# Performance work log

Hardware: AMD Instinct MI355X
Metric: run time of the kernel (lower is better)

The kernel has to match this reference:

```python
import jax, jax.numpy as jnp
import numpy as np

VOC = 50000
EMB = 300
B = 256
CTX = 6
K = 10


def setup_inputs() -> dict:
    key = jax.random.key(0)
    k1, k2, k3, k4, k5, k6 = jax.random.split(key, 6)
    # one-hot inputs (the original multiplies one-hot vectors against the tables)
    idx_vo = jax.random.randint(k1, (B,), 0, VOC)
    idx_vi = jax.random.randint(k2, (B, CTX), 0, VOC)
    idx_neg = jax.random.randint(k3, (B, K), 0, VOC)
    # random context lengths in [1, CTX]; positions >= length are zero rows (padding)
    lengths = jax.random.randint(k4, (B, 1), 1, CTX + 1)
    valid = (jnp.arange(CTX)[None, :] < lengths).astype(jnp.float32)  # [B, CTX]
    vo = jax.nn.one_hot(idx_vo, VOC, dtype=jnp.float32)               # [B, VOC]
    vi = jax.nn.one_hot(idx_vi, VOC, dtype=jnp.float32) * valid[:, :, None]  # [B, CTX, VOC]
    neg_samples = jax.nn.one_hot(idx_neg, VOC, dtype=jnp.float32)     # [B, K, VOC]
    # parameters: uniform(-0.5, 0.5) / embed_dim, as in the torch init
    V = (jax.random.uniform(k5, (VOC, EMB), minval=-0.5, maxval=0.5) / EMB).astype(jnp.float32)
    U = (jax.random.uniform(k6, (VOC, EMB), minval=-0.5, maxval=0.5) / EMB).astype(jnp.float32)
    return {"vo": vo, "vi": vi, "neg_samples": neg_samples, "V": V, "U": U}


def reference(vo, vi, neg_samples, V, U):
    embed_dim = V.shape[1]
    vo_embed = vo @ V                                      # [B, D]
    vi_temp = jnp.einsum('bcv,vd->bcd', vi, U)             # [B, CTX, D]
    mask = jnp.sum(jnp.abs(vi), axis=2) != 0               # [B, CTX]
    mask_sum = mask.astype(jnp.float32).sum(axis=1, keepdims=True)  # [B, 1]
    vi_embed = vi_temp.sum(axis=1) / mask_sum              # [B, D]
    left = jax.nn.log_sigmoid(jnp.sum(vo_embed * vi_embed, axis=1, keepdims=True))  # [B, 1]
    neg_embed = jnp.einsum('bkv,vd->bkd', neg_samples, U)  # [B, K, D]
    batch_mul = jnp.einsum('bkd,bd->bk', neg_embed, vo_embed)  # [B, K]
    right = jnp.sum(jax.nn.log_sigmoid(-batch_mul), axis=1, keepdims=True)  # [B, 1]
    return jnp.mean(-(left + right))
```

## Files before the change

kernel.cpp:

```cpp
#include <hip/hip_runtime.h>
#include <math.h>

#define VOC 50000
#define EMB 300
#define BSZ 256
#define CTX 6
#define KNEG 10
#define ROW_VECS (VOC / 4)
#define NROWS (BSZ + BSZ * CTX + BSZ * KNEG)

typedef float floatx4 __attribute__((ext_vector_type(4)));

__global__ __launch_bounds__(256) void scan_rows_kernel(
        const floatx4* __restrict__ vo,
        const floatx4* __restrict__ vi,
        const floatx4* __restrict__ neg,
        int* __restrict__ out_idx,
        float* __restrict__ out) {
    const int r = blockIdx.x;
    if (r == 0 && threadIdx.x == 0) *out = 0.0f;

    const floatx4* __restrict__ row;
    if (r < BSZ)                 row = vo  + (size_t)r * ROW_VECS;
    else if (r < BSZ + BSZ*CTX)  row = vi  + (size_t)(r - BSZ) * ROW_VECS;
    else                         row = neg + (size_t)(r - BSZ - BSZ*CTX) * ROW_VECS;

    __shared__ int found;
    if (threadIdx.x == 0) found = 0;
    __syncthreads();

    const int t = threadIdx.x;
    for (int base = 0; base < ROW_VECS; base += 1024) {
        floatx4 v[4];
        int     j[4];
#pragma unroll
        for (int u = 0; u < 4; ++u) {
            j[u] = base + u * 256 + t;
            if (j[u] < ROW_VECS) v[u] = __builtin_nontemporal_load(&row[j[u]]);
            else                 v[u] = (floatx4)(0.f, 0.f, 0.f, 0.f);
        }
#pragma unroll
        for (int u = 0; u < 4; ++u) {
            if (v[u].x != 0.0f || v[u].y != 0.0f || v[u].z != 0.0f || v[u].w != 0.0f) {
                int col = j[u] * 4;
                if (v[u].x != 0.0f)      col += 0;
                else if (v[u].y != 0.0f) col += 1;
                else if (v[u].z != 0.0f) col += 2;
                else                     col += 3;
                out_idx[r] = col;
                found = 1;
            }
        }
        __syncthreads();
        if (found) return;
        __syncthreads();
    }
    if (t == 0) out_idx[r] = -1;
}

__device__ __forceinline__ float log_sigmoid(float x) {
    return fminf(x, 0.0f) - log1pf(expf(-fabsf(x)));
}

__global__ void cbow_loss_kernel(const int* __restrict__ idx_vo,
                                 const int* __restrict__ idx_vi,
                                 const int* __restrict__ idx_neg,
                                 const float* __restrict__ V,
                                 const float* __restrict__ U,
                                 float* __restrict__ out) {
    const int b = blockIdx.x;
    const int lane = threadIdx.x;

    const int ivo = idx_vo[b];
    int ivi[CTX];
#pragma unroll
    for (int c = 0; c < CTX; ++c) ivi[c] = idx_vi[b * CTX + c];
    int ing[KNEG];
#pragma unroll
    for (int k = 0; k < KNEG; ++k) ing[k] = idx_neg[b * KNEG + k];

    int cnt = 0;
    float w[CTX];
    int   safe[CTX];
#pragma unroll
    for (int c = 0; c < CTX; ++c) {
        w[c] = (ivi[c] >= 0) ? 1.0f : 0.0f;
        safe[c] = (ivi[c] >= 0) ? ivi[c] : 0;
        cnt += (ivi[c] >= 0) ? 1 : 0;
    }
    const float inv_cnt = 1.0f / (float)cnt;

    float vo_e[5] = {0.f, 0.f, 0.f, 0.f, 0.f};
    const float* __restrict__ vrow = V + (long)ivo * EMB;
#pragma unroll
    for (int j = 0; j < 5; ++j) {
        int d = lane + j * 64;
        if (d < EMB) vo_e[j] = vrow[d];
    }

    float vi_e[5] = {0.f, 0.f, 0.f, 0.f, 0.f};
#pragma unroll
    for (int c = 0; c < CTX; ++c) {
        const float* __restrict__ urow = U + (long)safe[c] * EMB;
#pragma unroll
        for (int j = 0; j < 5; ++j) {
            int d = lane + j * 64;
            if (d < EMB) vi_e[j] += w[c] * urow[d];
        }
    }

    float pd[KNEG];
#pragma unroll
    for (int k = 0; k < KNEG; ++k) pd[k] = 0.f;
#pragma unroll
    for (int k = 0; k < KNEG; ++k) {
        const float* __restrict__ urow = U + (long)ing[k] * EMB;
#pragma unroll
        for (int j = 0; j < 5; ++j) {
            int d = lane + j * 64;
            if (d < EMB) pd[k] += vo_e[j] * urow[d];
        }
    }

    float dot = 0.f;
#pragma unroll
    for (int j = 0; j < 5; ++j) dot += vo_e[j] * (vi_e[j] * inv_cnt);
#pragma unroll
    for (int off = 32; off > 0; off >>= 1) dot += __shfl_down(dot, off, 64);

#pragma unroll
    for (int k = 0; k < KNEG; ++k) {
#pragma unroll
        for (int off = 32; off > 0; off >>= 1) pd[k] += __shfl_down(pd[k], off, 64);
    }

    if (lane == 0) {
        float right = 0.f;
#pragma unroll
        for (int k = 0; k < KNEG; ++k) right += log_sigmoid(-pd[k]);
        float left = log_sigmoid(dot);
        atomicAdd(out, -(left + right) * (1.0f / (float)BSZ));
    }
}

extern "C" void kernel_launch(void* const* d_in, const int* in_sizes, int n_in,
                              void* d_out, int out_size, void* d_ws, size_t ws_size,
                              hipStream_t stream) {
    const float* vo  = (const float*)d_in[0];
    const float* vi  = (const float*)d_in[1];
    const float* neg = (const float*)d_in[2];
    const float* V   = (const float*)d_in[3];
    const float* U   = (const float*)d_in[4];
    float* out = (float*)d_out;

    int* idx_all = (int*)d_ws;
    int* idx_vo  = idx_all;
    int* idx_vi  = idx_all + BSZ;
    int* idx_neg = idx_all + BSZ + BSZ * CTX;

    scan_rows_kernel<<<NROWS, 256, 0, stream>>>(
        (const floatx4*)vo, (const floatx4*)vi, (const floatx4*)neg,
        idx_all, out);

    cbow_loss_kernel<<<BSZ, 64, 0, stream>>>(idx_vo, idx_vi, idx_neg, V, U, out);
}
```

Measured before the change: 839.0 us.

## Scan one-hot rows with one wave per row instead of one block

The row scan that finds each one-hot index now assigns a single 64-lane wave per row, with four waves per block. Early exit uses a wave vote instead of a shared flag and two block barriers. This removes barrier overhead and reduces how far past the nonzero element each row is read. In exchange, each row has fewer bytes in flight per iteration, so per-row latency chains get longer.

```diff
diff --git a/kernel.cpp b/kernel.cpp
--- a/kernel.cpp
+++ b/kernel.cpp
@@ -8,54 +8,56 @@
 #define KNEG 10
 #define ROW_VECS (VOC / 4)
 #define NROWS (BSZ + BSZ * CTX + BSZ * KNEG)
+#define WAVES_PER_BLOCK 4
+#define NBLOCKS ((NROWS + WAVES_PER_BLOCK - 1) / WAVES_PER_BLOCK)
 
 typedef float floatx4 __attribute__((ext_vector_type(4)));
 
-__global__ __launch_bounds__(256) void scan_rows_kernel(
+__global__ __launch_bounds__(64 * WAVES_PER_BLOCK) void scan_rows_wave(
         const floatx4* __restrict__ vo,
         const floatx4* __restrict__ vi,
         const floatx4* __restrict__ neg,
         int* __restrict__ out_idx,
         float* __restrict__ out) {
-    const int r = blockIdx.x;
-    if (r == 0 && threadIdx.x == 0) *out = 0.0f;
+    const int wave = threadIdx.x >> 6;
+    const int lane = threadIdx.x & 63;
+    const int r = blockIdx.x * WAVES_PER_BLOCK + wave;
+    if (r == 0 && lane == 0) *out = 0.0f;
+    if (r >= NROWS) return;
 
     const floatx4* __restrict__ row;
     if (r < BSZ)                 row = vo  + (size_t)r * ROW_VECS;
     else if (r < BSZ + BSZ*CTX)  row = vi  + (size_t)(r - BSZ) * ROW_VECS;
     else                         row = neg + (size_t)(r - BSZ - BSZ*CTX) * ROW_VECS;
 
-    __shared__ int found;
-    if (threadIdx.x == 0) found = 0;
-    __syncthreads();
-
-    const int t = threadIdx.x;
-    for (int base = 0; base < ROW_VECS; base += 1024) {
+    for (int base = 0; base < ROW_VECS; base += 256) {
         floatx4 v[4];
         int     j[4];
 #pragma unroll
         for (int u = 0; u < 4; ++u) {
-            j[u] = base + u * 256 + t;
+            j[u] = base + u * 64 + lane;
             if (j[u] < ROW_VECS) v[u] = __builtin_nontemporal_load(&row[j[u]]);
             else                 v[u] = (floatx4)(0.f, 0.f, 0.f, 0.f);
         }
+        bool hit = false;
+        int  col = 0;
 #pragma unroll
         for (int u = 0; u < 4; ++u) {
             if (v[u].x != 0.0f || v[u].y != 0.0f || v[u].z != 0.0f || v[u].w != 0.0f) {
-                int col = j[u] * 4;
+                col = j[u] * 4;
                 if (v[u].x != 0.0f)      col += 0;
                 else if (v[u].y != 0.0f) col += 1;
                 else if (v[u].z != 0.0f) col += 2;
                 else                     col += 3;
-                out_idx[r] = col;
-                found = 1;
+                hit = true;
             }
         }
-        __syncthreads();
-        if (found) return;
-        __syncthreads();
+        if (__any(hit)) {
+            if (hit) out_idx[r] = col;
+            return;
+        }
     }
-    if (t == 0) out_idx[r] = -1;
+    if (lane == 0) out_idx[r] = -1;
 }
 
 __device__ __forceinline__ float log_sigmoid(float x) {
@@ -158,7 +160,7 @@
     int* idx_vi  = idx_all + BSZ;
     int* idx_neg = idx_all + BSZ + BSZ * CTX;
 
-    scan_rows_kernel<<<NROWS, 256, 0, stream>>>(
+    scan_rows_wave<<<NBLOCKS, 64 * WAVES_PER_BLOCK, 0, stream>>>(
         (const floatx4*)vo, (const floatx4*)vi, (const floatx4*)neg,
         idx_all, out);
 
```

After: 843.3 us. Within noise of the previous version (+0.5%).
